# Optimization experiments

Hardware: AMD Instinct MI355X
Metric: run time of the kernel (lower is better)

Reference implementation:

```python
import jax, jax.numpy as jnp
import numpy as np

B, S, E = 2, 2048, 2048
H, D = 16, 128           # n_heads, head_dim (= rope_dim)
BASE = 10000.0


def _rope_tables(seq_len, dim):
    inv_freq = 1.0 / (BASE ** (jnp.arange(0, dim, 2, dtype=jnp.float32) / dim))
    t = jnp.arange(seq_len, dtype=jnp.float32)
    freqs = jnp.outer(t, inv_freq)                 # [S, D/2]
    emb = jnp.concatenate([freqs, freqs], axis=-1)  # [S, D]
    cos = jnp.cos(emb)[None, :, None, :]            # [1, S, 1, D]
    sin = jnp.sin(emb)[None, :, None, :]
    return cos, sin


def _rotate_half(x):
    x1, x2 = x[..., : x.shape[-1] // 2], x[..., x.shape[-1] // 2:]
    return jnp.concatenate([-x2, x1], axis=-1)


def setup_inputs() -> dict:
    key = jax.random.key(0)
    ks = jax.random.split(key, 9)
    s = 1.0 / np.sqrt(E)
    return {
        "x": jax.random.normal(ks[0], (B, S, E), dtype=jnp.float32),
        "Wq": jax.random.uniform(ks[1], (E, E), jnp.float32, -s, s),
        "bq": jax.random.uniform(ks[2], (E,), jnp.float32, -s, s),
        "Wk": jax.random.uniform(ks[3], (E, E), jnp.float32, -s, s),
        "bk": jax.random.uniform(ks[4], (E,), jnp.float32, -s, s),
        "Wv": jax.random.uniform(ks[5], (E, E), jnp.float32, -s, s),
        "bv": jax.random.uniform(ks[6], (E,), jnp.float32, -s, s),
        "Wp": jax.random.uniform(ks[7], (E, E), jnp.float32, -s, s),
        "bp": jax.random.uniform(ks[8], (E,), jnp.float32, -s, s),
    }


def reference(x, Wq, bq, Wk, bk, Wv, bv, Wp, bp):
    b, s, e = x.shape
    # QKV projections (torch Linear: y = x W^T + b)
    q = (jnp.einsum("bse,fe->bsf", x, Wq) + bq).reshape(b, s, H, D)
    k = (jnp.einsum("bse,fe->bsf", x, Wk) + bk).reshape(b, s, H, D)
    v = (jnp.einsum("bse,fe->bsf", x, Wv) + bv).reshape(b, s, H, D)
    # RoPE (rope_dim == head_dim, start_pos = 0)
    cos, sin = _rope_tables(s, D)
    q = q * cos + _rotate_half(q) * sin
    k = k * cos + _rotate_half(k) * sin
    # attention scores [b, m, n, h]
    att = jnp.einsum("bmhd,bnhd->bmnh", q, k)
    causal = jnp.tril(jnp.ones((s, s), dtype=bool))[None, :, :, None]
    att = jnp.where(causal, att, -jnp.inf)
    att = jax.nn.softmax(att / np.sqrt(D), axis=2)
    out = jnp.einsum("bmnh,bnhd->bmhd", att, v).reshape(b, s, e)
    return jnp.einsum("bse,fe->bsf", out, Wp) + bp
```

## Files before the change

### kernel.cpp

```cpp
#include <hip/hip_runtime.h>
#include <hip/hip_bf16.h>
#include <math.h>

#define BB 2
#define SS 2048
#define EE 2048
#define HH 16
#define DD 128
#define MM (BB*SS)

typedef __attribute__((ext_vector_type(8))) short bf16x8;
typedef __attribute__((ext_vector_type(4))) float f32x4;
typedef __attribute__((ext_vector_type(16))) float f32x16;
typedef __attribute__((ext_vector_type(4))) unsigned u32x4;

__device__ inline float bf2f(const __hip_bfloat16 h){ return __bfloat162float(h); }
__device__ inline __hip_bfloat16 f2bf(float f){ return __float2bfloat16(f); }
__device__ inline short f2bs(float f){
  union { __hip_bfloat16 h; short s; } u; u.h = __float2bfloat16(f); return u.s;
}
__device__ inline unsigned pk2(float a, float b){
  union { __hip_bfloat162 h2; unsigned u; } x;
  x.h2 = __float22bfloat162_rn(float2{a,b}); return x.u;
}

__device__ inline void gload16(const void* g, void* l){
  __builtin_amdgcn_global_load_lds((const __attribute__((address_space(1))) void*)g,
      (__attribute__((address_space(3))) void*)l, 16, 0, 0);
}

#define QSCL 0.12754614533018515f

struct P5 { const float* s0; const float* s1; const float* s2; const float* s3; const float* s4;
            __hip_bfloat16* d0; __hip_bfloat16* d1; __hip_bfloat16* d2; __hip_bfloat16* d3; __hip_bfloat16* d4;
            int n0; int n1; };
__global__ void cvt5_kernel(P5 p){
  int w = blockIdx.y;
  const float* in = w==0 ? p.s0 : w==1 ? p.s1 : w==2 ? p.s2 : w==3 ? p.s3 : p.s4;
  __hip_bfloat16* out = w==0 ? p.d0 : w==1 ? p.d1 : w==2 ? p.d2 : w==3 ? p.d3 : p.d4;
  int n4 = w==0 ? p.n0 : p.n1;
  int i = blockIdx.x*256 + threadIdx.x;
  if (i >= n4) return;
  float4 v = ((const float4*)in)[i];
  union { short4 s4; short s[4]; } u;
  u.s[0] = f2bs(v.x); u.s[1] = f2bs(v.y); u.s[2] = f2bs(v.z); u.s[3] = f2bs(v.w);
  ((short4*)out)[i] = u.s4;
}

__global__ void rope_tables_kernel(float* __restrict__ cost, float* __restrict__ sint){
  int idx = blockIdx.x*256 + threadIdx.x;
  int s = idx >> 6, i = idx & 63;
  double inv = exp(-log(10000.0) * (double)i / 64.0);
  double f = (double)s * inv;
  cost[idx] = (float)cos(f);
  sint[idx] = (float)sin(f);
}

template<int MODE>
__global__ __launch_bounds__(512) void gemm256(const __hip_bfloat16* __restrict__ A,
        const __hip_bfloat16* __restrict__ Bw, const float* __restrict__ bias,
        void* __restrict__ Cout,
        const float* __restrict__ cost, const float* __restrict__ sint){
  __shared__ __align__(1024) char lds[147456];
  const int tid = threadIdx.x, wid = tid>>6, lane = tid&63, g = lane>>4, c16 = lane&15;
  const int wm = wid>>2, wn = wid&3;
  const int orig = blockIdx.x;
  const int wg = (orig & 7)*32 + (orig >> 3);
  const int bm = wg & 31, bn = wg >> 5;
  const int rowA0 = bm*128, rowB0 = bn*256;
  const char* Ab8 = (const char*)A + (size_t)rowA0*4096;
  const char* Bb8 = (const char*)Bw + (size_t)rowB0*4096;

  f32x4 acc[4][4] = {};

  auto stageA = [&](int t, char* buf, int i){
    int off = i*8192 + tid*16;
    int r = off >> 7;
    int cs = (off & 127) ^ ((r&7)<<4);
    gload16(Ab8 + (size_t)r*4096 + t*128 + cs, buf + i*8192 + wid*1024);
  };
  auto stageB = [&](int t, char* buf, int i){
    int off = i*8192 + tid*16;
    int r = off >> 7;
    int cs = (off & 127) ^ ((r&7)<<4);
    gload16(Bb8 + (size_t)r*4096 + t*128 + cs, buf + 16384 + i*8192 + wid*1024);
  };

  char* b0 = lds;
  char* b1 = lds + 49152;
  char* b2 = lds + 98304;

  stageA(0,b0,0); stageA(0,b0,1);
  stageB(0,b0,0); stageB(0,b0,1); stageB(0,b0,2); stageB(0,b0,3);
  stageA(1,b1,0); stageA(1,b1,1);
  stageB(1,b1,0); stageB(1,b1,1); stageB(1,b1,2); stageB(1,b1,3);
  asm volatile("s_waitcnt vmcnt(6)" ::: "memory");
  asm volatile("s_barrier" ::: "memory");

  const int rB[4] = { wn*64 + 0*16 + c16, wn*64 + 1*16 + c16, wn*64 + 2*16 + c16, wn*64 + 3*16 + c16 };
  const int rA[4] = { wm*64 + 0*16 + c16, wm*64 + 1*16 + c16, wm*64 + 2*16 + c16, wm*64 + 3*16 + c16 };

  #pragma unroll 1
  for (int t = 0; t < 32; ++t){
    const char* Abuf = b0;
    const char* Bbuf = b0 + 16384;
    const bool st = (t + 2 < 32);
    bf16x8 bfr[4];

    {
      #pragma unroll
      for (int ni=0;ni<4;ni++)
        bfr[ni] = *(const bf16x8*)(Bbuf + rB[ni]*128 + ((g*16) ^ ((rB[ni]&7)<<4)));
      bf16x8 a0 = *(const bf16x8*)(Abuf + rA[0]*128 + ((g*16) ^ ((rA[0]&7)<<4)));
      bf16x8 a1 = *(const bf16x8*)(Abuf + rA[1]*128 + ((g*16) ^ ((rA[1]&7)<<4)));
      if (st){ stageA(t+2,b2,0); stageA(t+2,b2,1); }
      asm volatile("s_barrier" ::: "memory");
      __builtin_amdgcn_s_setprio(1);
      #pragma unroll
      for (int ni=0;ni<4;ni++){
        acc[0][ni] = __builtin_amdgcn_mfma_f32_16x16x32_bf16(a0, bfr[ni], acc[0][ni],0,0,0);
        acc[1][ni] = __builtin_amdgcn_mfma_f32_16x16x32_bf16(a1, bfr[ni], acc[1][ni],0,0,0);
      }
      __builtin_amdgcn_s_setprio(0);
      asm volatile("s_barrier" ::: "memory");
    }
    {
      bf16x8 a2 = *(const bf16x8*)(Abuf + rA[2]*128 + ((g*16) ^ ((rA[2]&7)<<4)));
      bf16x8 a3 = *(const bf16x8*)(Abuf + rA[3]*128 + ((g*16) ^ ((rA[3]&7)<<4)));
      if (st){ stageB(t+2,b2,0); stageB(t+2,b2,1); }
      asm volatile("s_barrier" ::: "memory");
      __builtin_amdgcn_s_setprio(1);
      #pragma unroll
      for (int ni=0;ni<4;ni++){
        acc[2][ni] = __builtin_amdgcn_mfma_f32_16x16x32_bf16(a2, bfr[ni], acc[2][ni],0,0,0);
        acc[3][ni] = __builtin_amdgcn_mfma_f32_16x16x32_bf16(a3, bfr[ni], acc[3][ni],0,0,0);
      }
      __builtin_amdgcn_s_setprio(0);
      asm volatile("s_barrier" ::: "memory");
    }
    {
      #pragma unroll
      for (int ni=0;ni<4;ni++)
        bfr[ni] = *(const bf16x8*)(Bbuf + rB[ni]*128 + ((64 + g*16) ^ ((rB[ni]&7)<<4)));
      bf16x8 a0 = *(const bf16x8*)(Abuf + rA[0]*128 + ((64 + g*16) ^ ((rA[0]&7)<<4)));
      bf16x8 a1 = *(const bf16x8*)(Abuf + rA[1]*128 + ((64 + g*16) ^ ((rA[1]&7)<<4)));
      if (st){ stageB(t+2,b2,2); }
      asm volatile("s_barrier" ::: "memory");
      __builtin_amdgcn_s_setprio(1);
      #pragma unroll
      for (int ni=0;ni<4;ni++){
        acc[0][ni] = __builtin_amdgcn_mfma_f32_16x16x32_bf16(a0, bfr[ni], acc[0][ni],0,0,0);
        acc[1][ni] = __builtin_amdgcn_mfma_f32_16x16x32_bf16(a1, bfr[ni], acc[1][ni],0,0,0);
      }
      __builtin_amdgcn_s_setprio(0);
      asm volatile("s_barrier" ::: "memory");
    }
    {
      bf16x8 a2 = *(const bf16x8*)(Abuf + rA[2]*128 + ((64 + g*16) ^ ((rA[2]&7)<<4)));
      bf16x8 a3 = *(const bf16x8*)(Abuf + rA[3]*128 + ((64 + g*16) ^ ((rA[3]&7)<<4)));
      if (st){ stageB(t+2,b2,3); }
      asm volatile("s_barrier" ::: "memory");
      __builtin_amdgcn_s_setprio(1);
      #pragma unroll
      for (int ni=0;ni<4;ni++){
        acc[2][ni] = __builtin_amdgcn_mfma_f32_16x16x32_bf16(a2, bfr[ni], acc[2][ni],0,0,0);
        acc[3][ni] = __builtin_amdgcn_mfma_f32_16x16x32_bf16(a3, bfr[ni], acc[3][ni],0,0,0);
      }
      __builtin_amdgcn_s_setprio(0);
      if (t + 1 < 32){
        if (st) asm volatile("s_waitcnt vmcnt(6)" ::: "memory");
        else    asm volatile("s_waitcnt vmcnt(0)" ::: "memory");
      }
      asm volatile("s_barrier" ::: "memory");
    }
    char* tmp = b0; b0 = b1; b1 = b2; b2 = tmp;
  }

  if constexpr (MODE == 3 || MODE == 4){
    float* lf = (float*)lds;
    #pragma unroll
    for (int mi=0;mi<4;mi++){
      #pragma unroll
      for (int ni=0;ni<4;ni++){
        int fl = wn*64 + ni*16 + c16;
        float bv = bias[rowB0 + fl];
        #pragma unroll
        for (int j=0;j<4;j++){
          int ml = wm*64 + mi*16 + g*4 + j;
          lf[ml*260 + fl] = acc[mi][ni][j] + bv;
        }
      }
    }
    __syncthreads();
    #pragma unroll
    for (int mi=0;mi<4;mi++){
      #pragma unroll
      for (int ni=0;ni<4;ni++){
        int fl = wn*64 + ni*16 + c16;
        int f  = rowB0 + fl;
        float bv = bias[f];
        int i  = fl & 63;
        #pragma unroll
        for (int j=0;j<4;j++){
          int ml = wm*64 + mi*16 + g*4 + j;
          int m  = rowA0 + ml;
          int spos = m & (SS-1);
          float c  = cost[spos*64 + i];
          float sn = sint[spos*64 + i];
          float self = acc[mi][ni][j] + bv;
          float part = lf[ml*260 + (fl ^ 64)];
          float v = (fl & 64) ? (self*c + part*sn) : (self*c - part*sn);
          if constexpr (MODE == 3) v *= QSCL;
          ((__hip_bfloat16*)Cout)[(size_t)m*EE + f] = f2bf(v);
        }
      }
    }
  } else {
    #pragma unroll
    for (int mi=0;mi<4;mi++){
      #pragma unroll
      for (int ni=0;ni<4;ni++){
        int f = rowB0 + wn*64 + ni*16 + c16;
        float bv = bias[f];
        #pragma unroll
        for (int j=0;j<4;j++){
          int m = rowA0 + wm*64 + mi*16 + g*4 + j;
          float v = acc[mi][ni][j] + bv;
          if constexpr (MODE == 0) {
            ((__hip_bfloat16*)Cout)[(size_t)m*EE + f] = f2bf(v);
          } else if constexpr (MODE == 1) {
            int b = m >> 11, s = m & (SS-1);
            ((__hip_bfloat16*)Cout)[((size_t)(b*EE + f))*SS + s] = f2bf(v);
          } else {
            ((float*)Cout)[(size_t)m*EE + f] = v;
          }
        }
      }
    }
  }
}

__global__ __launch_bounds__(256, 2) void attn_kernel(const __hip_bfloat16* __restrict__ qg,
    const __hip_bfloat16* __restrict__ kg, const __hip_bfloat16* __restrict__ vtg,
    __hip_bfloat16* __restrict__ og){
  __shared__ short Ks[2][64*128];
  __shared__ short Vs3[3][64*128];
  const int tid=threadIdx.x, wid=tid>>6, lane=tid&63;
  const int c32 = lane & 31, hi = lane >> 5;
  const bool skew = (wid >= 2);
  const int id = blockIdx.x;
  const int u = id & 255;
  const int bh = u & 31, pr = u >> 5;
  const int qtile = (id < 256) ? (15 - pr) : pr;
  const int b = bh >> 4, h = bh & 15;
  const int q0 = qtile*128, qw = q0 + wid*32;
  const int qglob = qw + c32;
  const int niter = 2*qtile + 2;

  const char* kb8 = (const char*)(kg + ((size_t)b*SS)*EE + h*DD);
  const char* vb8 = (const char*)(vtg + (size_t)bh*DD*SS);

  const char* qrow = (const char*)(qg + ((size_t)(b*SS + qglob))*EE + h*DD);
  bf16x8 qf[8];
  #pragma unroll
  for (int s=0;s<8;s++) qf[s] = *(const bf16x8*)(qrow + s*32 + hi*16);

  f32x16 pacc[4] = {};
  float mrun = -INFINITY, lrun = 0.f;
  bf16x8 pf[4];

  auto stageK = [&](int kv, short* dst){
    #pragma unroll
    for (int i=0;i<4;i++){
      int base = i*4096 + wid*1024;
      int lb = base + lane*16;
      int r = lb >> 8, cb = lb & 255;
      gload16(kb8 + (size_t)(kv + r)*4096 + (cb ^ ((r&15)<<4)), (char*)dst + base);
    }
  };
  auto stageV = [&](int kv, short* dst){
    #pragma unroll
    for (int i=0;i<4;i++){
      int base = i*4096 + wid*1024;
      int lb = base + lane*16;
      int r = lb >> 8;
      int cs = (lb & 255) ^ ((r&15)<<4);
      int dsrc = r + ((cs >> 7) << 6);
      int kcol = cs & 127;
      gload16(vb8 + (size_t)dsrc*4096 + (size_t)kv*2 + kcol, (char*)dst + base);
    }
  };
  auto pvadd = [&](const short* vbuf){
    const char* Vb = (const char*)vbuf;
    __builtin_amdgcn_s_setprio(1);
    #pragma unroll
    for (int ds=0; ds<4; ds++){
      int d = ds*32 + c32;
      int rr = d & 63;
      int half = (d >> 6) << 7;
      const char* vr = Vb + rr*256;
      int vsw = (rr&15) << 4;
      #pragma unroll
      for (int ks=0; ks<4; ks++){
        bf16x8 vf = *(const bf16x8*)(vr + ((half + ks*32 + hi*16) ^ vsw));
        pacc[ds] = __builtin_amdgcn_mfma_f32_32x32x16_bf16(vf, pf[ks], pacc[ds], 0,0,0);
      }
    }
    __builtin_amdgcn_s_setprio(0);
  };

  short* va = Vs3[0]; short* vbuf = Vs3[1]; short* vc = Vs3[2];
  short* kc = Ks[0];  short* kn = Ks[1];

  stageK(0, kc); stageV(0, vbuf);
  __syncthreads();

  #pragma unroll 1
  for (int it = 0; it < niter; ++it){
    const int kv0 = it*64;
    if (it + 1 < niter){ stageK(kv0+64, kn); stageV(kv0+64, vc); }

    if (skew && it > 0) pvadd(va);

    const bool fullmask = (kv0 > qw + 31);
    if (!fullmask){
      f32x16 st0 = {}, st1 = {};
      {
        const char* Kb = (const char*)kc;
        __builtin_amdgcn_s_setprio(1);
        const int sw0 = (c32&15) << 4;
        #pragma unroll
        for (int s=0;s<8;s++){
          bf16x8 kf0 = *(const bf16x8*)(Kb + c32*256      + ((s*32 + hi*16) ^ sw0));
          bf16x8 kf1 = *(const bf16x8*)(Kb + (32+c32)*256 + ((s*32 + hi*16) ^ sw0));
          st0 = __builtin_amdgcn_mfma_f32_32x32x16_bf16(kf0, qf[s], st0, 0,0,0);
          st1 = __builtin_amdgcn_mfma_f32_32x32x16_bf16(kf1, qf[s], st1, 0,0,0);
        }
        __builtin_amdgcn_s_setprio(0);
      }

      float p[32];
      float vmax = -INFINITY;
      const bool domask = (kv0 + 63 > qw);
      #pragma unroll
      for (int r=0;r<16;r++){
        float v0 = st0[r], v1 = st1[r];
        if (domask){
          int kvo = (r&3) + 8*(r>>2) + 4*hi;
          if (kv0 + kvo > qglob)      v0 = -INFINITY;
          if (kv0 + 32 + kvo > qglob) v1 = -INFINITY;
        }
        p[r] = v0; p[16+r] = v1;
        vmax = fmaxf(vmax, fmaxf(v0, v1));
      }
      vmax = fmaxf(vmax, __shfl_xor(vmax, 32));

      const bool rescale = !__all(vmax <= mrun + 8.0f);
      float mnew = mrun;
      if (rescale){
        mnew = fmaxf(mrun, vmax);
        const float rs = exp2f(mrun - mnew);
        mrun = mnew;
        lrun *= rs;
        #pragma unroll
        for (int ds=0; ds<4; ds++)
          #pragma unroll
          for (int r=0;r<16;r++) pacc[ds][r] *= rs;
      }

      float s0=0.f, s1=0.f, s2=0.f, s3=0.f;
      #pragma unroll
      for (int i=0;i<8;i++){
        p[i]    = exp2f(p[i]    - mnew); s0 += p[i];
        p[8+i]  = exp2f(p[8+i]  - mnew); s1 += p[8+i];
        p[16+i] = exp2f(p[16+i] - mnew); s2 += p[16+i];
        p[24+i] = exp2f(p[24+i] - mnew); s3 += p[24+i];
      }
      float ps = (s0 + s1) + (s2 + s3);
      ps += __shfl_xor(ps, 32);
      lrun += ps;

      unsigned w[2][4][2];
      #pragma unroll
      for (int T=0;T<2;T++)
        #pragma unroll
        for (int m=0;m<4;m++)
          #pragma unroll
          for (int uu=0;uu<2;uu++)
            w[T][m][uu] = pk2(p[T*16 + 4*m + 2*uu], p[T*16 + 4*m + 2*uu + 1]);

      #pragma unroll
      for (int ks=0; ks<4; ks++){
        int T = ks>>1, lo2 = (ks&1)*2;
        unsigned o0 = hi ? w[T][lo2+1][0] : w[T][lo2+0][0];
        unsigned o1 = hi ? w[T][lo2+1][1] : w[T][lo2+0][1];
        unsigned x0 = hi ? w[T][lo2+0][0] : w[T][lo2+1][0];
        unsigned x1 = hi ? w[T][lo2+0][1] : w[T][lo2+1][1];
        unsigned r0 = (unsigned)__shfl_xor((int)x0, 32);
        unsigned r1 = (unsigned)__shfl_xor((int)x1, 32);
        union { u32x4 u4; bf16x8 h8; } cvt;
        cvt.u4[0] = hi ? r0 : o0;
        cvt.u4[1] = hi ? r1 : o1;
        cvt.u4[2] = hi ? o0 : r0;
        cvt.u4[3] = hi ? o1 : r1;
        pf[ks] = cvt.h8;
      }

      if (!skew) pvadd(vbuf);
    }

    __syncthreads();
    short* t = va; va = vbuf; vbuf = vc; vc = t;
    short* tk = kc; kc = kn; kn = tk;
  }

  if (skew) pvadd(va);

  const float invl = 1.0f / lrun;
  char* orow = (char*)(og + ((size_t)(b*SS + qglob))*EE + h*DD);
  #pragma unroll
  for (int ds=0; ds<4; ds++){
    #pragma unroll
    for (int m=0;m<4;m++){
      int d0 = ds*32 + 8*m + 4*hi;
      short4 s4;
      s4.x = f2bs(pacc[ds][4*m+0]*invl);
      s4.y = f2bs(pacc[ds][4*m+1]*invl);
      s4.z = f2bs(pacc[ds][4*m+2]*invl);
      s4.w = f2bs(pacc[ds][4*m+3]*invl);
      *(short4*)(orow + d0*2) = s4;
    }
  }
}

extern "C" void kernel_launch(void* const* d_in, const int* in_sizes, int n_in,
                              void* d_out, int out_size, void* d_ws, size_t ws_size,
                              hipStream_t stream){
  const float* x  = (const float*)d_in[0];
  const float* Wq = (const float*)d_in[1];
  const float* bq = (const float*)d_in[2];
  const float* Wk = (const float*)d_in[3];
  const float* bk = (const float*)d_in[4];
  const float* Wv = (const float*)d_in[5];
  const float* bv = (const float*)d_in[6];
  const float* Wp = (const float*)d_in[7];
  const float* bp = (const float*)d_in[8];
  float* out = (float*)d_out;

  char* ws = (char*)d_ws;
  size_t off = 0;
  auto alloc = [&](size_t bytes){ void* p = ws + off; off += (bytes + 255) & ~(size_t)255; return p; };
  const size_t nx = (size_t)MM*EE;
  const size_t nw = (size_t)EE*EE;
  __hip_bfloat16* xb  = (__hip_bfloat16*)alloc(nx*2);
  __hip_bfloat16* wqb = (__hip_bfloat16*)alloc(nw*2);
  __hip_bfloat16* wkb = (__hip_bfloat16*)alloc(nw*2);
  __hip_bfloat16* wvb = (__hip_bfloat16*)alloc(nw*2);
  __hip_bfloat16* wpb = (__hip_bfloat16*)alloc(nw*2);
  __hip_bfloat16* qb  = (__hip_bfloat16*)alloc(nx*2);
  __hip_bfloat16* kb  = (__hip_bfloat16*)alloc(nx*2);
  __hip_bfloat16* vtb = (__hip_bfloat16*)alloc(nx*2);
  __hip_bfloat16* ob  = (__hip_bfloat16*)alloc(nx*2);
  float* cost = (float*)alloc((size_t)SS*64*4);
  float* sint = (float*)alloc((size_t)SS*64*4);

  P5 p5{x, Wq, Wk, Wv, Wp, xb, wqb, wkb, wvb, wpb, (int)(nx/4), (int)(nw/4)};
  cvt5_kernel<<<dim3((int)(nx/4/256), 5), 256, 0, stream>>>(p5);
  rope_tables_kernel<<<SS*64/256, 256, 0, stream>>>(cost, sint);

  gemm256<3><<<256, 512, 0, stream>>>(xb, wqb, bq, qb,  cost, sint);
  gemm256<4><<<256, 512, 0, stream>>>(xb, wkb, bk, kb,  cost, sint);
  gemm256<1><<<256, 512, 0, stream>>>(xb, wvb, bv, vtb, nullptr, nullptr);

  attn_kernel<<<dim3(512), 256, 0, stream>>>(qb, kb, vtb, ob);

  gemm256<2><<<256, 512, 0, stream>>>(ob, wpb, bp, out, nullptr, nullptr);
}
```

Before: 263.2 us.

## Merge GEMM k-tile phases into two full 4x4 MFMA phases and vectorize transposed store

Restructures the GEMM main loop to process two k-tiles per iteration. Each k-tile now runs two phases, each loading all A and B fragments and issuing the full 4x4 MFMA block, instead of four phases of 2x4. This halves the number of barriers and groups global staging into two halves per tile. The transposed-output (MODE 1) epilogue now packs four consecutive bf16 values into one short4 store instead of four scattered 2-byte stores. In exchange, more fragment registers are live at once, and the buffer rotation logic becomes more complex.

```diff
diff --git a/kernel.cpp b/kernel.cpp
--- a/kernel.cpp
+++ b/kernel.cpp
@@ -85,95 +85,60 @@
     int cs = (off & 127) ^ ((r&7)<<4);
     gload16(Bb8 + (size_t)r*4096 + t*128 + cs, buf + 16384 + i*8192 + wid*1024);
   };
+  auto stageH1 = [&](int t, char* buf){ stageA(t,buf,0); stageA(t,buf,1); stageB(t,buf,0); };
+  auto stageH2 = [&](int t, char* buf){ stageB(t,buf,1); stageB(t,buf,2); stageB(t,buf,3); };
 
   char* b0 = lds;
   char* b1 = lds + 49152;
   char* b2 = lds + 98304;
 
-  stageA(0,b0,0); stageA(0,b0,1);
-  stageB(0,b0,0); stageB(0,b0,1); stageB(0,b0,2); stageB(0,b0,3);
-  stageA(1,b1,0); stageA(1,b1,1);
-  stageB(1,b1,0); stageB(1,b1,1); stageB(1,b1,2); stageB(1,b1,3);
+  stageH1(0,b0); stageH2(0,b0);
+  stageH1(1,b1); stageH2(1,b1);
   asm volatile("s_waitcnt vmcnt(6)" ::: "memory");
   asm volatile("s_barrier" ::: "memory");
 
   const int rB[4] = { wn*64 + 0*16 + c16, wn*64 + 1*16 + c16, wn*64 + 2*16 + c16, wn*64 + 3*16 + c16 };
   const int rA[4] = { wm*64 + 0*16 + c16, wm*64 + 1*16 + c16, wm*64 + 2*16 + c16, wm*64 + 3*16 + c16 };
 
+  auto phase = [&](const char* buf, int kk, int stT, char* stBuf, int stHalf, int wcnt){
+    const char* Abuf = buf;
+    const char* Bbuf = buf + 16384;
+    bf16x8 bfr[4], af[4];
+    #pragma unroll
+    for (int ni=0;ni<4;ni++)
+      bfr[ni] = *(const bf16x8*)(Bbuf + rB[ni]*128 + ((kk + g*16) ^ ((rB[ni]&7)<<4)));
+    #pragma unroll
+    for (int mi=0;mi<4;mi++)
+      af[mi] = *(const bf16x8*)(Abuf + rA[mi]*128 + ((kk + g*16) ^ ((rA[mi]&7)<<4)));
+    if (stT >= 0){ if (stHalf == 0) stageH1(stT, stBuf); else stageH2(stT, stBuf); }
+    asm volatile("s_barrier" ::: "memory");
+    __builtin_amdgcn_s_setprio(1);
+    #pragma unroll
+    for (int mi=0;mi<4;mi++)
+      #pragma unroll
+      for (int ni=0;ni<4;ni++)
+        acc[mi][ni] = __builtin_amdgcn_mfma_f32_16x16x32_bf16(af[mi], bfr[ni], acc[mi][ni],0,0,0);
+    __builtin_amdgcn_s_setprio(0);
+    if (wcnt == 6)      asm volatile("s_waitcnt vmcnt(6)" ::: "memory");
+    else if (wcnt == 0) asm volatile("s_waitcnt vmcnt(0)" ::: "memory");
+    asm volatile("s_barrier" ::: "memory");
+  };
+
   #pragma unroll 1
-  for (int t = 0; t < 32; ++t){
-    const char* Abuf = b0;
-    const char* Bbuf = b0 + 16384;
-    const bool st = (t + 2 < 32);
-    bf16x8 bfr[4];
-
-    {
-      #pragma unroll
-      for (int ni=0;ni<4;ni++)
-        bfr[ni] = *(const bf16x8*)(Bbuf + rB[ni]*128 + ((g*16) ^ ((rB[ni]&7)<<4)));
-      bf16x8 a0 = *(const bf16x8*)(Abuf + rA[0]*128 + ((g*16) ^ ((rA[0]&7)<<4)));
-      bf16x8 a1 = *(const bf16x8*)(Abuf + rA[1]*128 + ((g*16) ^ ((rA[1]&7)<<4)));
-      if (st){ stageA(t+2,b2,0); stageA(t+2,b2,1); }
-      asm volatile("s_barrier" ::: "memory");
-      __builtin_amdgcn_s_setprio(1);
-      #pragma unroll
-      for (int ni=0;ni<4;ni++){
-        acc[0][ni] = __builtin_amdgcn_mfma_f32_16x16x32_bf16(a0, bfr[ni], acc[0][ni],0,0,0);
-        acc[1][ni] = __builtin_amdgcn_mfma_f32_16x16x32_bf16(a1, bfr[ni], acc[1][ni],0,0,0);
-      }
-      __builtin_amdgcn_s_setprio(0);
-      asm volatile("s_barrier" ::: "memory");
-    }
-    {
-      bf16x8 a2 = *(const bf16x8*)(Abuf + rA[2]*128 + ((g*16) ^ ((rA[2]&7)<<4)));
-      bf16x8 a3 = *(const bf16x8*)(Abuf + rA[3]*128 + ((g*16) ^ ((rA[3]&7)<<4)));
-      if (st){ stageB(t+2,b2,0); stageB(t+2,b2,1); }
-      asm volatile("s_barrier" ::: "memory");
-      __builtin_amdgcn_s_setprio(1);
-      #pragma unroll
-      for (int ni=0;ni<4;ni++){
-        acc[2][ni] = __builtin_amdgcn_mfma_f32_16x16x32_bf16(a2, bfr[ni], acc[2][ni],0,0,0);
-        acc[3][ni] = __builtin_amdgcn_mfma_f32_16x16x32_bf16(a3, bfr[ni], acc[3][ni],0,0,0);
-      }
-      __builtin_amdgcn_s_setprio(0);
-      asm volatile("s_barrier" ::: "memory");
-    }
-    {
-      #pragma unroll
-      for (int ni=0;ni<4;ni++)
-        bfr[ni] = *(const bf16x8*)(Bbuf + rB[ni]*128 + ((64 + g*16) ^ ((rB[ni]&7)<<4)));
-      bf16x8 a0 = *(const bf16x8*)(Abuf + rA[0]*128 + ((64 + g*16) ^ ((rA[0]&7)<<4)));
-      bf16x8 a1 = *(const bf16x8*)(Abuf + rA[1]*128 + ((64 + g*16) ^ ((rA[1]&7)<<4)));
-      if (st){ stageB(t+2,b2,2); }
-      asm volatile("s_barrier" ::: "memory");
-      __builtin_amdgcn_s_setprio(1);
-      #pragma unroll
-      for (int ni=0;ni<4;ni++){
-        acc[0][ni] = __builtin_amdgcn_mfma_f32_16x16x32_bf16(a0, bfr[ni], acc[0][ni],0,0,0);
-        acc[1][ni] = __builtin_amdgcn_mfma_f32_16x16x32_bf16(a1, bfr[ni], acc[1][ni],0,0,0);
-      }
-      __builtin_amdgcn_s_setprio(0);
-      asm volatile("s_barrier" ::: "memory");
-    }
-    {
-      bf16x8 a2 = *(const bf16x8*)(Abuf + rA[2]*128 + ((64 + g*16) ^ ((rA[2]&7)<<4)));
-      bf16x8 a3 = *(const bf16x8*)(Abuf + rA[3]*128 + ((64 + g*16) ^ ((rA[3]&7)<<4)));
-      if (st){ stageB(t+2,b2,3); }
-      asm volatile("s_barrier" ::: "memory");
-      __builtin_amdgcn_s_setprio(1);
-      #pragma unroll
-      for (int ni=0;ni<4;ni++){
-        acc[2][ni] = __builtin_amdgcn_mfma_f32_16x16x32_bf16(a2, bfr[ni], acc[2][ni],0,0,0);
-        acc[3][ni] = __builtin_amdgcn_mfma_f32_16x16x32_bf16(a3, bfr[ni], acc[3][ni],0,0,0);
-      }
-      __builtin_amdgcn_s_setprio(0);
-      if (t + 1 < 32){
-        if (st) asm volatile("s_waitcnt vmcnt(6)" ::: "memory");
-        else    asm volatile("s_waitcnt vmcnt(0)" ::: "memory");
-      }
-      asm volatile("s_barrier" ::: "memory");
-    }
-    char* tmp = b0; b0 = b1; b1 = b2; b2 = tmp;
+  for (int t = 0; t < 32; t += 2){
+    const bool s2 = (t + 2 < 32);
+    const bool s3 = (t + 3 < 32);
+    phase(b0, 0,  s2 ? t+2 : -1, b2, 0, -1);
+    phase(b0, 64, s2 ? t+2 : -1, b2, 1, s2 ? 6 : 0);
+    phase(b1, 0,  s3 ? t+3 : -1, b0, 0, -1);
+    phase(b1, 64, s3 ? t+3 : -1, b0, 1, s3 ? 6 : (s2 ? 0 : -1));
+    char* ob0 = b0;
+    b0 = b2; b1 = ob0; b2 = lds + ((b2 == lds ? 49152 : (b2 == lds+49152 ? 98304 : 0)));
+    b2 = ob0 == lds ? ( (lds+49152 == b0) ? lds+98304 : lds+49152 ) : b2;
+    char* all0 = lds; char* all1 = lds+49152; char* all2 = lds+98304;
+    if ((b0==all0&&b1==all1)||(b0==all1&&b1==all0)) b2=all2;
+    else if ((b0==all0&&b1==all2)||(b0==all2&&b1==all0)) b2=all1;
+    else b2=all0;
   }
 
   if constexpr (MODE == 3 || MODE == 4){
@@ -215,6 +180,23 @@
         }
       }
     }
+  } else if constexpr (MODE == 1){
+    #pragma unroll
+    for (int mi=0;mi<4;mi++){
+      #pragma unroll
+      for (int ni=0;ni<4;ni++){
+        int f = rowB0 + wn*64 + ni*16 + c16;
+        float bv = bias[f];
+        int m0 = rowA0 + wm*64 + mi*16 + g*4;
+        int b = m0 >> 11, s0 = m0 & (SS-1);
+        short4 s4;
+        s4.x = f2bs(acc[mi][ni][0] + bv);
+        s4.y = f2bs(acc[mi][ni][1] + bv);
+        s4.z = f2bs(acc[mi][ni][2] + bv);
+        s4.w = f2bs(acc[mi][ni][3] + bv);
+        *(short4*)&((__hip_bfloat16*)Cout)[((size_t)(b*EE + f))*SS + s0] = s4;
+      }
+    }
   } else {
     #pragma unroll
     for (int mi=0;mi<4;mi++){
@@ -228,9 +210,6 @@
           float v = acc[mi][ni][j] + bv;
           if constexpr (MODE == 0) {
             ((__hip_bfloat16*)Cout)[(size_t)m*EE + f] = f2bf(v);
-          } else if constexpr (MODE == 1) {
-            int b = m >> 11, s = m & (SS-1);
-            ((__hip_bfloat16*)Cout)[((size_t)(b*EE + f))*SS + s] = f2bf(v);
           } else {
             ((float*)Cout)[(size_t)m*EE + f] = v;
           }
```

After: 263.7 us. Within noise of the previous version (+0.2%).
